# Kernel tuning notes

Hardware: AMD Instinct MI355X
Metric: run time of the kernel (lower is better)

Reference implementation:

```python
import jax, jax.numpy as jnp
import numpy as np
from jax import lax

STRIDE = 4
SCALES = (32.0, 64.0, 128.0)
RATIOS = (0.5, 1.0, 2.0)
PRE_NMS = 6000          # pre_nms_top_n['testing']
POST_NMS = 1000         # post_nms_top_n['testing']
NMS_THRESH = 0.7
MIN_SIZE = 1.0


def make_anchors(fh, fw):
    # 9 base anchors per cell (3 scales x 3 ratios), xyxy centered at cell centers.
    base = []
    for s in SCALES:
        for r in RATIOS:
            w = s * np.sqrt(1.0 / r)
            h = s * np.sqrt(r)
            base.append([-w / 2, -h / 2, w / 2, h / 2])
    base = np.asarray(base, np.float32)                      # [9,4]
    xs = (np.arange(fw, dtype=np.float32) + 0.5) * STRIDE
    ys = (np.arange(fh, dtype=np.float32) + 0.5) * STRIDE
    cx, cy = np.meshgrid(xs, ys)                             # [fh,fw]
    shifts = np.stack([cx, cy, cx, cy], -1)[:, :, None, :]   # [fh,fw,1,4]
    return jnp.asarray((shifts + base[None, None]).reshape(-1, 4))  # [fh*fw*9,4]


def conv(x, w, b):
    y = lax.conv_general_dilated(x, w, (1, 1), 'SAME',
                                 dimension_numbers=('NCHW', 'OIHW', 'NCHW'))
    return y + b[None, :, None, None]


def decode(anchors, deltas):
    wa = anchors[:, 2] - anchors[:, 0]
    ha = anchors[:, 3] - anchors[:, 1]
    cxa = anchors[:, 0] + 0.5 * wa
    cya = anchors[:, 1] + 0.5 * ha
    cx = deltas[:, 0] * wa + cxa
    cy = deltas[:, 1] * ha + cya
    w = jnp.exp(deltas[:, 2]) * wa
    h = jnp.exp(deltas[:, 3]) * ha
    return jnp.stack([cx - 0.5 * w, cy - 0.5 * h, cx + 0.5 * w, cy + 0.5 * h], -1)


def pairwise_iou(a, b):
    area_a = (a[:, 2] - a[:, 0]) * (a[:, 3] - a[:, 1])
    area_b = (b[:, 2] - b[:, 0]) * (b[:, 3] - b[:, 1])
    lt = jnp.maximum(a[:, None, :2], b[None, :, :2])
    rb = jnp.minimum(a[:, None, 2:], b[None, :, 2:])
    wh = jnp.clip(rb - lt, 0.0)
    inter = wh[..., 0] * wh[..., 1]
    return inter / (area_a[:, None] + area_b[None, :] - inter + 1e-9)


def nms_keep(boxes, valid, thresh):
    # boxes already sorted by score descending; greedy suppression.
    n = boxes.shape[0]
    iou = pairwise_iou(boxes, boxes)  # [n,n]
    def body(i, keep):
        suppressed = jnp.any((iou[i] > thresh) & keep)
        return keep.at[i].set(valid[i] & ~suppressed)
    return lax.fori_loop(0, n, body, jnp.zeros(n, bool))


def rpn_forward(feature, w1, b1, w_cls, b_cls, w_reg, b_reg, image_h, image_w,
                detach_for_proposal=True):
    fh, fw = feature.shape[2], feature.shape[3]
    x = jax.nn.relu(conv(feature, w1, b1))
    conf = conv(x, w_cls, b_cls).transpose(0, 2, 3, 1).reshape(-1)        # [N]
    offsets = conv(x, w_reg, b_reg).transpose(0, 2, 3, 1).reshape(-1, 4)  # [N,4]
    if detach_for_proposal:  # original detaches before create_proposal
        conf = lax.stop_gradient(conf)
        offsets = lax.stop_gradient(offsets)
    anchors = make_anchors(fh, fw)

    pre_n = min(PRE_NMS, conf.shape[0])
    scores, idx = lax.top_k(conf, pre_n)
    props = decode(anchors[idx], offsets[idx])
    # process_box: clip to image, drop boxes smaller than min_size (mask form)
    props = jnp.stack([jnp.clip(props[:, 0], 0.0, float(image_w)),
                       jnp.clip(props[:, 1], 0.0, float(image_h)),
                       jnp.clip(props[:, 2], 0.0, float(image_w)),
                       jnp.clip(props[:, 3], 0.0, float(image_h))], -1)
    valid = ((props[:, 2] - props[:, 0]) >= MIN_SIZE) & \
            ((props[:, 3] - props[:, 1]) >= MIN_SIZE)

    keep = nms_keep(lax.stop_gradient(props), valid, NMS_THRESH)
    # compact first POST_NMS kept boxes into a fixed-shape output (zero padded)
    rank = jnp.cumsum(keep) - 1
    dest = jnp.where(keep & (rank < POST_NMS), rank, POST_NMS)
    out = jnp.zeros((POST_NMS + 1, 4), props.dtype).at[dest].set(props)[:POST_NMS]
    return out


def setup_inputs() -> dict:
    key = jax.random.key(0)
    ks = jax.random.split(key, 4)
    return {
        'feature': jax.random.normal(ks[0], (1, 256, 200, 272), jnp.float32),
        'w1': jax.random.normal(ks[1], (256, 256, 3, 3), jnp.float32) * 0.02,
        'b1': jnp.zeros((256,), jnp.float32),
        'w_cls': jax.random.normal(ks[2], (9, 256, 1, 1), jnp.float32) * 0.02,
        'b_cls': jnp.zeros((9,), jnp.float32),
        'w_reg': jax.random.normal(ks[3], (36, 256, 1, 1), jnp.float32) * 0.01,
        'b_reg': jnp.zeros((36,), jnp.float32),
        'image_h': 800,
        'image_w': 1088,
    }


def reference(feature, w1, b1, w_cls, b_cls, w_reg, b_reg, image_h, image_w):
    return rpn_forward(feature, w1, b1, w_cls, b_cls, w_reg, b_reg,
                       image_h, image_w, detach_for_proposal=True)
```

## Files before the change

### kernel.cpp

```cpp
#include <hip/hip_runtime.h>
#include <hip/hip_bf16.h>
#include <math.h>

#define H_ 200
#define W_ 272
#define C_ 256
#define HW 54400
#define NANCH 489600
#define PRE_N 6000
#define POST_N 1000
#define NWORDS 94
#define CHUNK_W 2720

#define X_OFF       0ull
#define CONF_OFF    55705600ull
#define HIST1_OFF   57664000ull
#define HIST2_OFF   57926144ull
#define SCAL_OFF    58188288ull
#define SEL_OFF     58188544ull
#define TOPIDX_OFF  58254080ull
#define BOXES_OFF   58278080ull
#define VALID_OFF   58374080ull
#define MASK_OFF    58398080ull
#define W1R_OFF     62910080ull
#define WCR_OFF     65269376ull

__device__ __forceinline__ unsigned fkey(float fv) {
    unsigned u = __float_as_uint(fv);
    return (u & 0x80000000u) ? ~u : (u | 0x80000000u);
}

__global__ __launch_bounds__(256) void k_init(const float* __restrict__ w1,
                                              const float* __restrict__ wcls,
                                              unsigned* __restrict__ hist1,
                                              float* __restrict__ w1r,
                                              float* __restrict__ wcr) {
    int e = blockIdx.x * 256 + threadIdx.x;
    if (e < 131136) hist1[e] = 0u;
    int e1 = e - 131136;
    if (e1 >= 0 && e1 < 589824) {
        int oc = e1 / 2304; int rem = e1 % 2304; int ic = rem / 9; int k = rem % 9;
        int wg = oc >> 3, o = oc & 7;
        w1r[(((size_t)wg * 256 + ic) * 9 + k) * 8 + o] = w1[e1];
    } else if (e1 >= 589824 && e1 < 589824 + 2304) {
        int e2 = e1 - 589824; int a = e2 / 256; int c = e2 % 256;
        wcr[c * 9 + a] = wcls[e2];
    }
}

__global__ __launch_bounds__(256, 4) void k_conv1(const float* __restrict__ f,
                                                  const float* __restrict__ w1r,
                                                  const float* __restrict__ b1,
                                                  float* __restrict__ xo) {
    __shared__ __align__(16) float sI[8 * 10 * 36];
    int tid = threadIdx.x;
    int lane = tid & 63;
    int wgl = __builtin_amdgcn_readfirstlane(tid >> 6);
    int xg = lane & 7;
    int yg = lane >> 3;
    int X0 = blockIdx.x * 32;
    int Y0 = blockIdx.y * 8;
    int wg = blockIdx.z * 4 + wgl;
    int y = Y0 + yg;
    int xbase = X0 + xg * 4;

    int off[11]; int lds[11]; bool ok[11];
#pragma unroll
    for (int it = 0; it < 11; it++) {
        int l = tid + it * 256;
        int ci = l / 340; int r = l - ci * 340; int ry = r / 34; int rx = r - ry * 34;
        int gx = X0 - 1 + rx, gy = Y0 - 1 + ry;
        ok[it] = (l < CHUNK_W) && gx >= 0 && gx < W_ && gy >= 0 && gy < H_;
        off[it] = ci * HW + gy * W_ + gx;
        lds[it] = (ci * 10 + ry) * 36 + rx;
    }
    float rbuf[11];
#pragma unroll
    for (int it = 0; it < 11; it++)
        rbuf[it] = ok[it] ? f[off[it]] : 0.f;

    float acc[8][4];
#pragma unroll
    for (int o = 0; o < 8; o++)
#pragma unroll
        for (int i = 0; i < 4; i++) acc[o][i] = 0.f;

    const float* wbase = w1r + (size_t)wg * 256 * 72;

    for (int ic0 = 0; ic0 < 256; ic0 += 8) {
        __syncthreads();
#pragma unroll
        for (int it = 0; it < 11; it++)
            if (tid + it * 256 < CHUNK_W) sI[lds[it]] = rbuf[it];
        __syncthreads();
        if (ic0 < 248) {
            const float* fn = f + (size_t)(ic0 + 8) * HW;
#pragma unroll
            for (int it = 0; it < 11; it++)
                rbuf[it] = ok[it] ? fn[off[it]] : 0.f;
        }
        for (int ci = 0; ci < 8; ci++) {
            const float* wp = wbase + (size_t)(ic0 + ci) * 72;
#pragma unroll
            for (int ky = 0; ky < 3; ky++) {
                const float* irow = &sI[(ci * 10 + yg + ky) * 36 + xg * 4];
                float in[6];
#pragma unroll
                for (int j = 0; j < 6; j++) in[j] = irow[j];
                const float* wrow = wp + ky * 24;
#pragma unroll
                for (int kx = 0; kx < 3; kx++) {
#pragma unroll
                    for (int o = 0; o < 8; o++) {
                        float w = wrow[kx * 8 + o];
#pragma unroll
                        for (int i = 0; i < 4; i++)
                            acc[o][i] = fmaf(w, in[i + kx], acc[o][i]);
                    }
                }
            }
        }
    }
#pragma unroll
    for (int o = 0; o < 8; o++) {
        int oc = wg * 8 + o;
        float bv = b1[oc];
        float* orow = xo + (size_t)oc * HW + y * W_ + xbase;
        float v0 = fmaxf(acc[o][0] + bv, 0.f), v1 = fmaxf(acc[o][1] + bv, 0.f);
        float v2 = fmaxf(acc[o][2] + bv, 0.f), v3 = fmaxf(acc[o][3] + bv, 0.f);
        if (xbase + 3 < W_) {
            *(float4*)orow = make_float4(v0, v1, v2, v3);
        } else {
            float vv[4] = {v0, v1, v2, v3};
            for (int i = 0; i < 4; i++)
                if (xbase + i < W_) orow[i] = vv[i];
        }
    }
}

__global__ __launch_bounds__(256) void k_cls(const float* __restrict__ x,
                                             const float* __restrict__ wcr,
                                             const float* __restrict__ bc,
                                             float* __restrict__ conf,
                                             unsigned* __restrict__ hist) {
    int p = blockIdx.x * 256 + threadIdx.x;
    if (p >= HW) return;
    float acc[9];
#pragma unroll
    for (int a = 0; a < 9; a++) acc[a] = 0.f;
    for (int c = 0; c < 256; c++) {
        float xv = x[c * HW + p];
        const float* wp = wcr + c * 9;
#pragma unroll
        for (int a = 0; a < 9; a++) acc[a] = fmaf(wp[a], xv, acc[a]);
    }
#pragma unroll
    for (int a = 0; a < 9; a++) {
        float v = acc[a] + bc[a];
        conf[p * 9 + a] = v;
        atomicAdd(&hist[fkey(v) >> 16], 1u);
    }
}

__global__ __launch_bounds__(256) void k_hist2(const float* __restrict__ conf,
                                               const unsigned* __restrict__ scal, unsigned* hist) {
    int n = blockIdx.x * 256 + threadIdx.x;
    if (n >= NANCH) return;
    unsigned key = fkey(conf[n]);
    if ((key >> 16) == scal[0]) atomicAdd(&hist[key & 0xFFFFu], 1u);
}

__global__ __launch_bounds__(1024) void k_scan(const unsigned* __restrict__ hist,
                                               unsigned* scal, int mode) {
    __shared__ unsigned ssum[1024];
    int t = threadIdx.x;
    unsigned target = 6000u - (mode ? scal[1] : 0u);
    int base = 65535 - t * 64;
    unsigned s = 0;
    for (int k = 0; k < 64; k++) s += hist[base - k];
    ssum[t] = s;
    __syncthreads();
    for (int off = 1; off < 1024; off <<= 1) {
        unsigned v = (t >= off) ? ssum[t - off] : 0u;
        __syncthreads();
        ssum[t] += v;
        __syncthreads();
    }
    unsigned incl = ssum[t], excl = incl - s;
    if (excl < target && target <= incl) {
        unsigned run = excl;
        for (int k = 0; k < 64; k++) {
            unsigned c = hist[base - k];
            if (run + c >= target) { scal[2 * mode] = (unsigned)(base - k); scal[2 * mode + 1] = run; break; }
            run += c;
        }
    }
}

__global__ __launch_bounds__(256) void k_gather(const float* __restrict__ conf,
                                                unsigned* scal, unsigned long long* sel) {
    int n = blockIdx.x * 256 + threadIdx.x;
    if (n >= NANCH) return;
    unsigned B1 = scal[0], cnt1 = scal[1], B2 = scal[2], cnt2 = scal[3];
    unsigned T = (B1 << 16) | B2;
    unsigned key = fkey(conf[n]);
    if (key < T) return;
    unsigned long long kk = ((unsigned long long)(~key) << 32) | (unsigned)n;
    if (key > T) {
        unsigned pos = atomicAdd(&scal[4], 1u);
        if (pos < 8192u) sel[pos] = kk;
    } else {
        unsigned pos = cnt1 + cnt2 + atomicAdd(&scal[5], 1u);
        if (pos < 8192u) sel[pos] = kk;
    }
}

__global__ __launch_bounds__(1024) void k_sort(const unsigned* __restrict__ scal,
                                               const unsigned long long* __restrict__ sel,
                                               unsigned* __restrict__ topidx) {
    __shared__ unsigned long long sk[8192];
    unsigned G = scal[1] + scal[3];
    unsigned filled = G + scal[5];
    if (filled > 8192u) filled = 8192u;
    for (int i = threadIdx.x; i < 8192; i += 1024)
        sk[i] = (i < (int)filled) ? sel[i] : 0xFFFFFFFFFFFFFFFFull;
    __syncthreads();
    for (int k = 2; k <= 8192; k <<= 1) {
        for (int j = k >> 1; j > 0; j >>= 1) {
            for (int i = threadIdx.x; i < 8192; i += 1024) {
                int l = i ^ j;
                if (l > i) {
                    unsigned long long a = sk[i], b = sk[l];
                    bool up = ((i & k) == 0);
                    if ((a > b) == up) { sk[i] = b; sk[l] = a; }
                }
            }
            __syncthreads();
        }
    }
    for (int r = threadIdx.x; r < PRE_N; r += 1024)
        topidx[r] = (unsigned)(sk[r] & 0xFFFFFFFFull);
}

__global__ __launch_bounds__(64) void k_prop(const float* __restrict__ x,
                                             const float* __restrict__ wreg,
                                             const float* __restrict__ breg,
                                             const unsigned* __restrict__ topidx,
                                             const int* __restrict__ imh, const int* __restrict__ imw,
                                             float* __restrict__ boxes, int* __restrict__ valid) {
    int r = blockIdx.x;
    int lane = threadIdx.x;
    unsigned n = topidx[r];
    int a = (int)(n % 9u); int p = (int)(n / 9u);
    const float* wr = wreg + (4 * a) * 256;
    float s0 = 0, s1 = 0, s2 = 0, s3 = 0;
    for (int c = lane; c < 256; c += 64) {
        float xv = x[c * HW + p];
        s0 = fmaf(wr[c], xv, s0);
        s1 = fmaf(wr[256 + c], xv, s1);
        s2 = fmaf(wr[512 + c], xv, s2);
        s3 = fmaf(wr[768 + c], xv, s3);
    }
#pragma unroll
    for (int off = 32; off >= 1; off >>= 1) {
        s0 += __shfl_down(s0, off);
        s1 += __shfl_down(s1, off);
        s2 += __shfl_down(s2, off);
        s3 += __shfl_down(s3, off);
    }
    if (lane == 0) {
        float dx = s0 + breg[4 * a], dy = s1 + breg[4 * a + 1];
        float dw = s2 + breg[4 * a + 2], dh = s3 + breg[4 * a + 3];
        int wi = p % W_, hi = p / W_;
        const double SC[3] = {32.0, 64.0, 128.0};
        const double RT[3] = {0.5, 1.0, 2.0};
        double sd = SC[a / 3], rd = RT[a % 3];
        double wb = sd * sqrt(1.0 / rd), hb = sd * sqrt(rd);
        float bx1 = (float)(-wb * 0.5), by1 = (float)(-hb * 0.5);
        float bx2 = (float)(wb * 0.5),  by2 = (float)(hb * 0.5);
        float cxs = ((float)wi + 0.5f) * 4.0f, cys = ((float)hi + 0.5f) * 4.0f;
        float x1a = cxs + bx1, y1a = cys + by1, x2a = cxs + bx2, y2a = cys + by2;
        float wa = x2a - x1a, ha = y2a - y1a;
        float cxa = x1a + 0.5f * wa, cya = y1a + 0.5f * ha;
        float cx = dx * wa + cxa, cy = dy * ha + cya;
        float ww = expf(dw) * wa, hh = expf(dh) * ha;
        float X1 = cx - 0.5f * ww, Y1 = cy - 0.5f * hh;
        float X2 = cx + 0.5f * ww, Y2 = cy + 0.5f * hh;
        float Wf = (float)(*imw), Hf = (float)(*imh);
        X1 = fminf(fmaxf(X1, 0.f), Wf); Y1 = fminf(fmaxf(Y1, 0.f), Hf);
        X2 = fminf(fmaxf(X2, 0.f), Wf); Y2 = fminf(fmaxf(Y2, 0.f), Hf);
        boxes[4 * r] = X1; boxes[4 * r + 1] = Y1; boxes[4 * r + 2] = X2; boxes[4 * r + 3] = Y2;
        valid[r] = ((X2 - X1) >= 1.0f && (Y2 - Y1) >= 1.0f) ? 1 : 0;
    }
}

__global__ __launch_bounds__(256) void k_mask(const float* __restrict__ boxes,
                                              unsigned long long* __restrict__ mask) {
    __shared__ float jb[256];
    int jw = blockIdx.x;
    int i = blockIdx.y * 256 + threadIdx.x;
    {
        int idx = jw * 256 + threadIdx.x;
        jb[threadIdx.x] = (idx < PRE_N * 4) ? boxes[idx] : 0.f;
    }
    __syncthreads();
    if (i >= PRE_N) return;
    float ax1 = boxes[4 * i], ay1 = boxes[4 * i + 1], ax2 = boxes[4 * i + 2], ay2 = boxes[4 * i + 3];
    float aarea = (ax2 - ax1) * (ay2 - ay1);
    unsigned long long m = 0;
    int jbase = jw * 64;
    for (int b = 0; b < 64; b++) {
        int j = jbase + b;
        if (j <= i || j >= PRE_N) continue;
        float bx1 = jb[4 * b], by1 = jb[4 * b + 1], bx2 = jb[4 * b + 2], by2 = jb[4 * b + 3];
        float barea = (bx2 - bx1) * (by2 - by1);
        float xx1 = fmaxf(ax1, bx1), yy1 = fmaxf(ay1, by1);
        float xx2 = fminf(ax2, bx2), yy2 = fminf(ay2, by2);
        float w = fmaxf(xx2 - xx1, 0.f), h = fmaxf(yy2 - yy1, 0.f);
        float inter = w * h;
        float iou = inter / (aarea + barea - inter + 1e-9f);
        if (iou > 0.7f) m |= (1ull << b);
    }
    mask[(size_t)i * NWORDS + jw] = m;
}

__global__ __launch_bounds__(128) void k_scan_nms(const unsigned long long* __restrict__ mask,
                                                  const int* __restrict__ valid,
                                                  const float* __restrict__ boxes,
                                                  float* __restrict__ out) {
    __shared__ unsigned long long diag[NWORDS][64];
    __shared__ unsigned long long removed[NWORDS];
    __shared__ unsigned long long validw[NWORDS];
    __shared__ int keepList[POST_N];
    __shared__ int cnt;
    __shared__ unsigned long long keptbits;
    int t = threadIdx.x;
    if (t < NWORDS) { removed[t] = 0ull; validw[t] = 0ull; }
    if (t == 0) cnt = 0;
    __syncthreads();
    for (int l = t; l < NWORDS * 64; l += 128) {
        int w = l >> 6, b = l & 63;
        int i = w * 64 + b;
        diag[w][b] = (i < PRE_N) ? mask[(size_t)i * NWORDS + w] : 0ull;
    }
    for (int i = t; i < PRE_N; i += 128)
        if (valid[i]) atomicOr(&validw[i >> 6], 1ull << (i & 63));
    __syncthreads();
    for (int w = 0; w < NWORDS; w++) {
        unsigned long long candw = validw[w] & ~removed[w];
        if (!candw) continue;
        if (t == 0) {
            unsigned long long cand = candw;
            unsigned long long kb = 0ull;
            int c = cnt;
            while (cand && c < POST_N) {
                int b = __ffsll((unsigned long long)cand) - 1;
                keepList[c++] = w * 64 + b;
                kb |= 1ull << b;
                cand &= ~(1ull << b);
                cand &= ~diag[w][b];
            }
            cnt = c; keptbits = kb;
        }
        __syncthreads();
        if (cnt >= POST_N) break;
        unsigned long long kb = keptbits;
        if (kb) {
            for (int w2 = w + 1 + t; w2 < NWORDS; w2 += 128) {
                unsigned long long acc2 = removed[w2];
                unsigned long long tt = kb;
                while (tt) {
                    int b = __ffsll((unsigned long long)tt) - 1;
                    tt &= tt - 1;
                    acc2 |= mask[(size_t)(w * 64 + b) * NWORDS + w2];
                }
                removed[w2] = acc2;
            }
        }
        __syncthreads();
    }
    __syncthreads();
    int c = cnt;
    for (int e = t; e < POST_N * 4; e += 128) {
        int r = e >> 2;
        out[e] = (r < c) ? boxes[4 * keepList[r] + (e & 3)] : 0.f;
    }
}

extern "C" void kernel_launch(void* const* d_in, const int* in_sizes, int n_in,
                              void* d_out, int out_size, void* d_ws, size_t ws_size,
                              hipStream_t stream) {
    const float* feature = (const float*)d_in[0];
    const float* w1   = (const float*)d_in[1];
    const float* b1   = (const float*)d_in[2];
    const float* wcls = (const float*)d_in[3];
    const float* bcls = (const float*)d_in[4];
    const float* wreg = (const float*)d_in[5];
    const float* breg = (const float*)d_in[6];
    const int* imh = (const int*)d_in[7];
    const int* imw = (const int*)d_in[8];

    char* ws = (char*)d_ws;
    float* xbuf  = (float*)(ws + X_OFF);
    float* conf  = (float*)(ws + CONF_OFF);
    unsigned* hist1 = (unsigned*)(ws + HIST1_OFF);
    unsigned* hist2 = (unsigned*)(ws + HIST2_OFF);
    unsigned* scal  = (unsigned*)(ws + SCAL_OFF);
    unsigned long long* sel = (unsigned long long*)(ws + SEL_OFF);
    unsigned* topidx = (unsigned*)(ws + TOPIDX_OFF);
    float* boxes = (float*)(ws + BOXES_OFF);
    int* valid   = (int*)(ws + VALID_OFF);
    unsigned long long* mask = (unsigned long long*)(ws + MASK_OFF);
    float* w1r = (float*)(ws + W1R_OFF);
    float* wcr = (float*)(ws + WCR_OFF);
    float* outF = (float*)d_out;

    hipLaunchKernelGGL(k_init,   dim3(2826), dim3(256), 0, stream, w1, wcls, hist1, w1r, wcr);
    hipLaunchKernelGGL(k_conv1,  dim3(9, 25, 8), dim3(256), 0, stream, feature, w1r, b1, xbuf);
    hipLaunchKernelGGL(k_cls,    dim3(213),  dim3(256), 0, stream, xbuf, wcr, bcls, conf, hist1);
    hipLaunchKernelGGL(k_scan,   dim3(1),    dim3(1024), 0, stream, hist1, scal, 0);
    hipLaunchKernelGGL(k_hist2,  dim3(1913), dim3(256), 0, stream, conf, scal, hist2);
    hipLaunchKernelGGL(k_scan,   dim3(1),    dim3(1024), 0, stream, hist2, scal, 1);
    hipLaunchKernelGGL(k_gather, dim3(1913), dim3(256), 0, stream, conf, scal, sel);
    hipLaunchKernelGGL(k_sort,   dim3(1),    dim3(1024), 0, stream, scal, sel, topidx);
    hipLaunchKernelGGL(k_prop,   dim3(PRE_N), dim3(64), 0, stream, xbuf, wreg, breg, topidx, imh, imw, boxes, valid);
    hipLaunchKernelGGL(k_mask,   dim3(NWORDS, 24), dim3(256), 0, stream, boxes, mask);
    hipLaunchKernelGGL(k_scan_nms, dim3(1), dim3(128), 0, stream, mask, valid, boxes, outF);
}
```

Baseline: 1.793 ms.

## Double-buffer conv input tile and replace single-block bitonic sort with parallel rank

The 3x3 conv kernel now ping-pongs between two shared-memory input buffers. This cuts one barrier per channel chunk, and it reads input rows with float4/float2 vector loads. The minBlocks hint of 4 in launch_bounds is dropped, which may change register allocation and occupancy. The single-block 1024-thread bitonic sort over 8192 keys is replaced by a 32-block rank-by-counting kernel: each key counts how many keys are smaller and scatters itself to that position. This spreads the sort across many CUs at the cost of quadratic compares, and relies on the keys being unique, which holds because the anchor index is embedded in each key.

```diff
diff --git a/kernel.cpp b/kernel.cpp
--- a/kernel.cpp
+++ b/kernel.cpp
@@ -48,11 +48,11 @@
     }
 }
 
-__global__ __launch_bounds__(256, 4) void k_conv1(const float* __restrict__ f,
-                                                  const float* __restrict__ w1r,
-                                                  const float* __restrict__ b1,
-                                                  float* __restrict__ xo) {
-    __shared__ __align__(16) float sI[8 * 10 * 36];
+__global__ __launch_bounds__(256) void k_conv1(const float* __restrict__ f,
+                                               const float* __restrict__ w1r,
+                                               const float* __restrict__ b1,
+                                               float* __restrict__ xo) {
+    __shared__ __align__(16) float sI[2][2880];
     int tid = threadIdx.x;
     int lane = tid & 63;
     int wgl = __builtin_amdgcn_readfirstlane(tid >> 6);
@@ -78,6 +78,10 @@
 #pragma unroll
     for (int it = 0; it < 11; it++)
         rbuf[it] = ok[it] ? f[off[it]] : 0.f;
+#pragma unroll
+    for (int it = 0; it < 11; it++)
+        if (tid + it * 256 < CHUNK_W) sI[0][lds[it]] = rbuf[it];
+    __syncthreads();
 
     float acc[8][4];
 #pragma unroll
@@ -87,26 +91,23 @@
 
     const float* wbase = w1r + (size_t)wg * 256 * 72;
 
+    int cur = 0;
     for (int ic0 = 0; ic0 < 256; ic0 += 8) {
-        __syncthreads();
-#pragma unroll
-        for (int it = 0; it < 11; it++)
-            if (tid + it * 256 < CHUNK_W) sI[lds[it]] = rbuf[it];
-        __syncthreads();
         if (ic0 < 248) {
             const float* fn = f + (size_t)(ic0 + 8) * HW;
 #pragma unroll
             for (int it = 0; it < 11; it++)
                 rbuf[it] = ok[it] ? fn[off[it]] : 0.f;
         }
+        const float* sbuf = sI[cur];
         for (int ci = 0; ci < 8; ci++) {
             const float* wp = wbase + (size_t)(ic0 + ci) * 72;
 #pragma unroll
             for (int ky = 0; ky < 3; ky++) {
-                const float* irow = &sI[(ci * 10 + yg + ky) * 36 + xg * 4];
-                float in[6];
-#pragma unroll
-                for (int j = 0; j < 6; j++) in[j] = irow[j];
+                const float* irow = &sbuf[(ci * 10 + yg + ky) * 36 + xg * 4];
+                float4 va = *(const float4*)irow;
+                float2 vb = *(const float2*)(irow + 4);
+                float in[6] = {va.x, va.y, va.z, va.w, vb.x, vb.y};
                 const float* wrow = wp + ky * 24;
 #pragma unroll
                 for (int kx = 0; kx < 3; kx++) {
@@ -120,6 +121,13 @@
                 }
             }
         }
+        if (ic0 < 248) {
+#pragma unroll
+            for (int it = 0; it < 11; it++)
+                if (tid + it * 256 < CHUNK_W) sI[cur ^ 1][lds[it]] = rbuf[it];
+        }
+        __syncthreads();
+        cur ^= 1;
     }
 #pragma unroll
     for (int o = 0; o < 8; o++) {
@@ -215,31 +223,31 @@
     }
 }
 
-__global__ __launch_bounds__(1024) void k_sort(const unsigned* __restrict__ scal,
-                                               const unsigned long long* __restrict__ sel,
-                                               unsigned* __restrict__ topidx) {
-    __shared__ unsigned long long sk[8192];
+__global__ __launch_bounds__(256) void k_rank(const unsigned* __restrict__ scal,
+                                              const unsigned long long* __restrict__ sel,
+                                              unsigned* __restrict__ topidx) {
+    __shared__ unsigned long long tile[2048];
     unsigned G = scal[1] + scal[3];
     unsigned filled = G + scal[5];
     if (filled > 8192u) filled = 8192u;
-    for (int i = threadIdx.x; i < 8192; i += 1024)
-        sk[i] = (i < (int)filled) ? sel[i] : 0xFFFFFFFFFFFFFFFFull;
-    __syncthreads();
-    for (int k = 2; k <= 8192; k <<= 1) {
-        for (int j = k >> 1; j > 0; j >>= 1) {
-            for (int i = threadIdx.x; i < 8192; i += 1024) {
-                int l = i ^ j;
-                if (l > i) {
-                    unsigned long long a = sk[i], b = sk[l];
-                    bool up = ((i & k) == 0);
-                    if ((a > b) == up) { sk[i] = b; sk[l] = a; }
-                }
-            }
-            __syncthreads();
-        }
-    }
-    for (int r = threadIdx.x; r < PRE_N; r += 1024)
-        topidx[r] = (unsigned)(sk[r] & 0xFFFFFFFFull);
+    int i = blockIdx.x * 256 + threadIdx.x;
+    unsigned long long mykey = (i < (int)filled) ? sel[i] : 0xFFFFFFFFFFFFFFFFull;
+    int rank = 0;
+    for (int t0 = 0; t0 < 8192; t0 += 2048) {
+        __syncthreads();
+        for (int l = threadIdx.x; l < 2048; l += 256) {
+            int j = t0 + l;
+            tile[l] = (j < (int)filled) ? sel[j] : 0xFFFFFFFFFFFFFFFFull;
+        }
+        __syncthreads();
+        for (int l = 0; l < 2048; l += 4) {
+            ulonglong2 p = *(const ulonglong2*)&tile[l];
+            ulonglong2 q = *(const ulonglong2*)&tile[l + 2];
+            rank += (p.x < mykey) + (p.y < mykey) + (q.x < mykey) + (q.y < mykey);
+        }
+    }
+    if (i < (int)filled && rank < PRE_N)
+        topidx[rank] = (unsigned)(mykey & 0xFFFFFFFFull);
 }
 
 __global__ __launch_bounds__(64) void k_prop(const float* __restrict__ x,
@@ -422,7 +430,7 @@
     hipLaunchKernelGGL(k_hist2,  dim3(1913), dim3(256), 0, stream, conf, scal, hist2);
     hipLaunchKernelGGL(k_scan,   dim3(1),    dim3(1024), 0, stream, hist2, scal, 1);
     hipLaunchKernelGGL(k_gather, dim3(1913), dim3(256), 0, stream, conf, scal, sel);
-    hipLaunchKernelGGL(k_sort,   dim3(1),    dim3(1024), 0, stream, scal, sel, topidx);
+    hipLaunchKernelGGL(k_rank,   dim3(32),   dim3(256), 0, stream, scal, sel, topidx);
     hipLaunchKernelGGL(k_prop,   dim3(PRE_N), dim3(64), 0, stream, xbuf, wreg, breg, topidx, imh, imw, boxes, valid);
     hipLaunchKernelGGL(k_mask,   dim3(NWORDS, 24), dim3(256), 0, stream, boxes, mask);
     hipLaunchKernelGGL(k_scan_nms, dim3(1), dim3(128), 0, stream, mask, valid, boxes, outF);
```

After: 1.594 ms. -11.1%, faster.
